# Optimization experiments

Measured on AMD Instinct MI355X. Metric: run time of the kernel, lower is better.

The kernel has to match this reference:

```python
import jax, jax.numpy as jnp
import numpy as np

B = 256          # batch
S = 128 * 128    # s = imwidth*imheight (flattened image)
R = 16           # TT rank
N = 6            # number of TT cores


def setup_inputs() -> dict:
    key = jax.random.key(0)
    ks = jax.random.split(key, N + 1)
    # layeroptions['normalize']: cores divided by sqrt(sqrt(s))
    scale = 0.02 / np.sqrt(np.sqrt(S))
    ranklist = [1] + [R] * (N - 1) + [1]
    inp = {"z": jax.random.normal(ks[0], (B, S), dtype=jnp.float32)}
    for n in range(N):
        inp[f"core{n}"] = (
            jax.random.normal(ks[n + 1], (ranklist[n], S, ranklist[n + 1]), dtype=jnp.float32)
            * scale
        )
    inp["b"] = B
    return inp


def reference(z, core0, core1, core2, core3, core4, core5, b):
    # cores[k] has shape (d1, S, d2) with ranklist = [1, R, ..., R, 1]
    cores = [core0, core1, core2, core3, core4, core5]
    # f starts as TT[0][0] : (S, R)  (first core has d1 == 1)
    f = core0[0]
    # V_k[b] = sum_s z[b, s] * cores[k][:, s, :]   -> (b, d1, d2)
    # (equivalent to matmul(z, TT[k].permute(1,0,2).reshape(S, d1*d2)))
    V1 = jnp.einsum('bs,dse->bde', z, cores[1])          # (B, R, R)
    f = jnp.einsum('sd,bde->bse', f, V1)                 # (B, S, R)
    for k in range(2, N):
        Vk = jnp.einsum('bs,dse->bde', z, cores[k])      # (B, R, d2)
        f = jnp.einsum('bsd,bde->bse', f, Vk)            # (B, S, d2)
    # final d2 == 1 -> (B, S, 1) -> flatten like f.reshape(-1)
    return f.reshape(-1)
```

## Files before the change

kernel.cpp:

```cpp
#include <hip/hip_runtime.h>
#include <cstddef>
#include <cstdint>

namespace {
constexpr int kB = 256;
constexpr int kS = 16384;
constexpr int kNCol = 1040;
constexpr int kSB = kS / 8;
}

using short8 = __attribute__((ext_vector_type(8))) short;
using f32x4  = __attribute__((ext_vector_type(4))) float;

__global__ __launch_bounds__(256) void fttv_split(
    const float* __restrict__ z,
    unsigned short* __restrict__ zh, unsigned short* __restrict__ zl)
{
    const int i = blockIdx.x * 256 + threadIdx.x;
    const int lr = i & 15;
    const int sblk = (i >> 4) & (kSB - 1);
    const int rowblk = i >> 15;
    const int row = rowblk * 16 + lr;
    const float* src = z + (size_t)row * kS + sblk * 8;
    float x[8];
    *reinterpret_cast<float4*>(&x[0]) = *reinterpret_cast<const float4*>(src);
    *reinterpret_cast<float4*>(&x[4]) = *reinterpret_cast<const float4*>(src + 4);
    short8 h, l;
    #pragma unroll
    for (int j = 0; j < 8; ++j) {
        const uint32_t u = __float_as_uint(x[j]);
        h[j] = (short)(u >> 16);
        const float r = x[j] - __uint_as_float(u & 0xffff0000u);
        l[j] = (short)(__float_as_uint(r) >> 16);
    }
    const size_t idx = (((size_t)rowblk * kSB + sblk) * 16 + lr) * 8;
    *reinterpret_cast<short8*>(zh + idx) = h;
    *reinterpret_cast<short8*>(zl + idx) = l;
}

__device__ __forceinline__ void load_a(
    const unsigned short* __restrict__ zhp, const unsigned short* __restrict__ zlp,
    int sblk0, short8 ah[4], short8 al[4])
{
    #pragma unroll
    for (int fm = 0; fm < 4; ++fm) {
        const size_t o = ((size_t)fm * kSB + sblk0) * 128;
        ah[fm] = *reinterpret_cast<const short8*>(zhp + o);
        al[fm] = *reinterpret_cast<const short8*>(zlp + o);
    }
}

__device__ __forceinline__ void load_b(const float* const bptr[4], int s0,
                                       float rb[4][8])
{
    #pragma unroll
    for (int fn = 0; fn < 4; ++fn)
        #pragma unroll
        for (int j = 0; j < 8; ++j)
            rb[fn][j] = bptr[fn][(size_t)(s0 + j) * 16];
}

__device__ __forceinline__ void step_mfma(
    const short8 ah[4], const short8 al[4], const float rb[4][8],
    f32x4 acc[4][4])
{
    #pragma unroll
    for (int fn = 0; fn < 4; ++fn) {
        short8 bh, bl;
        #pragma unroll
        for (int j = 0; j < 8; ++j) {
            const uint32_t u = __float_as_uint(rb[fn][j]);
            bh[j] = (short)(u >> 16);
            const float r = rb[fn][j] - __uint_as_float(u & 0xffff0000u);
            bl[j] = (short)(__float_as_uint(r) >> 16);
        }
        #pragma unroll
        for (int fm = 0; fm < 4; ++fm) {
            acc[fm][fn] = __builtin_amdgcn_mfma_f32_16x16x32_bf16(
                ah[fm], bh, acc[fm][fn], 0, 0, 0);
            acc[fm][fn] = __builtin_amdgcn_mfma_f32_16x16x32_bf16(
                ah[fm], bl, acc[fm][fn], 0, 0, 0);
            acc[fm][fn] = __builtin_amdgcn_mfma_f32_16x16x32_bf16(
                al[fm], bh, acc[fm][fn], 0, 0, 0);
        }
    }
}

__global__ __launch_bounds__(64, 2) void fttv_gemm_t(
    const unsigned short* __restrict__ zh, const unsigned short* __restrict__ zl,
    const float* __restrict__ c1, const float* __restrict__ c2,
    const float* __restrict__ c3, const float* __restrict__ c4,
    const float* __restrict__ c5,
    float* __restrict__ vp, int kc)
{
    const int nwg = gridDim.x;
    const int q = nwg >> 3, r = nwg & 7;
    const int xcd = blockIdx.x & 7, rest = blockIdx.x >> 3;
    const int vfl = (xcd < r ? xcd * (q + 1) : r * (q + 1) + (xcd - r) * q) + rest;
    const int sk = vfl / 68;
    const int rem = vfl - sk * 68;
    const int mt = rem / 17;
    const int cg = rem - mt * 17;

    const int l = threadIdx.x;
    const int lr = l & 15, lkq = l >> 4;
    const int nsteps = kc >> 5;
    const int sb00 = sk * (kc >> 3);
    const int s0base = sk * kc + lkq * 8;

    const unsigned short* zhp = zh + ((size_t)(mt * 4) * kSB + lkq) * 128 + lr * 8;
    const unsigned short* zlp = zl + ((size_t)(mt * 4) * kSB + lkq) * 128 + lr * 8;

    f32x4 acc[4][4];
    #pragma unroll
    for (int i = 0; i < 4; ++i)
        #pragma unroll
        for (int j = 0; j < 4; ++j) acc[i][j] = (f32x4){0.f, 0.f, 0.f, 0.f};

    short8 ah0[4], al0[4], ah1[4], al1[4];

    if (cg < 16) {
        const int ci = cg >> 2;
        const float* cp = (ci == 0 ? c1 : ci == 1 ? c2 : ci == 2 ? c3 : c4);
        const int d0 = (cg & 3) * 4;
        const float* bptr[4];
        #pragma unroll
        for (int fn = 0; fn < 4; ++fn)
            bptr[fn] = cp + (size_t)(d0 + fn) * kS * 16 + lr;

        float rb0[4][8], rb1[4][8];
        load_b(bptr, s0base, rb0);
        load_a(zhp, zlp, sb00, ah0, al0);
        for (int t = 0; t < nsteps; t += 2) {
            load_b(bptr, s0base + (t + 1) * 32, rb1);
            load_a(zhp, zlp, sb00 + (t + 1) * 4, ah1, al1);
            step_mfma(ah0, al0, rb0, acc);
            if (t + 2 < nsteps) {
                load_b(bptr, s0base + (t + 2) * 32, rb0);
                load_a(zhp, zlp, sb00 + (t + 2) * 4, ah0, al0);
            }
            step_mfma(ah1, al1, rb1, acc);
        }
        #pragma unroll
        for (int fm = 0; fm < 4; ++fm)
            #pragma unroll
            for (int fn = 0; fn < 4; ++fn) {
                const int col = cg * 64 + fn * 16 + lr;
                const int brow = mt * 64 + fm * 16 + lkq * 4;
                #pragma unroll
                for (int qq = 0; qq < 4; ++qq)
                    vp[((size_t)sk * kB + brow + qq) * kNCol + col] =
                        acc[fm][fn][qq];
            }
    } else {
        const float* bp5 = c5 + (size_t)lr * kS;
        float r50[8], r51[8];
        load_a(zhp, zlp, sb00, ah0, al0);
        *reinterpret_cast<float4*>(&r50[0]) =
            *reinterpret_cast<const float4*>(bp5 + s0base);
        *reinterpret_cast<float4*>(&r50[4]) =
            *reinterpret_cast<const float4*>(bp5 + s0base + 4);
        for (int t = 0; t < nsteps; t += 2) {
            load_a(zhp, zlp, sb00 + (t + 1) * 4, ah1, al1);
            *reinterpret_cast<float4*>(&r51[0]) =
                *reinterpret_cast<const float4*>(bp5 + s0base + (t + 1) * 32);
            *reinterpret_cast<float4*>(&r51[4]) =
                *reinterpret_cast<const float4*>(bp5 + s0base + (t + 1) * 32 + 4);
            {
                short8 bh, bl;
                #pragma unroll
                for (int j = 0; j < 8; ++j) {
                    const uint32_t u = __float_as_uint(r50[j]);
                    bh[j] = (short)(u >> 16);
                    const float rr = r50[j] - __uint_as_float(u & 0xffff0000u);
                    bl[j] = (short)(__float_as_uint(rr) >> 16);
                }
                #pragma unroll
                for (int fm = 0; fm < 4; ++fm) {
                    acc[fm][0] = __builtin_amdgcn_mfma_f32_16x16x32_bf16(
                        ah0[fm], bh, acc[fm][0], 0, 0, 0);
                    acc[fm][0] = __builtin_amdgcn_mfma_f32_16x16x32_bf16(
                        ah0[fm], bl, acc[fm][0], 0, 0, 0);
                    acc[fm][0] = __builtin_amdgcn_mfma_f32_16x16x32_bf16(
                        al0[fm], bh, acc[fm][0], 0, 0, 0);
                }
            }
            if (t + 2 < nsteps) {
                load_a(zhp, zlp, sb00 + (t + 2) * 4, ah0, al0);
                *reinterpret_cast<float4*>(&r50[0]) =
                    *reinterpret_cast<const float4*>(bp5 + s0base + (t + 2) * 32);
                *reinterpret_cast<float4*>(&r50[4]) =
                    *reinterpret_cast<const float4*>(bp5 + s0base + (t + 2) * 32 + 4);
            }
            {
                short8 bh, bl;
                #pragma unroll
                for (int j = 0; j < 8; ++j) {
                    const uint32_t u = __float_as_uint(r51[j]);
                    bh[j] = (short)(u >> 16);
                    const float rr = r51[j] - __uint_as_float(u & 0xffff0000u);
                    bl[j] = (short)(__float_as_uint(rr) >> 16);
                }
                #pragma unroll
                for (int fm = 0; fm < 4; ++fm) {
                    acc[fm][0] = __builtin_amdgcn_mfma_f32_16x16x32_bf16(
                        ah1[fm], bh, acc[fm][0], 0, 0, 0);
                    acc[fm][0] = __builtin_amdgcn_mfma_f32_16x16x32_bf16(
                        ah1[fm], bl, acc[fm][0], 0, 0, 0);
                    acc[fm][0] = __builtin_amdgcn_mfma_f32_16x16x32_bf16(
                        al1[fm], bh, acc[fm][0], 0, 0, 0);
                }
            }
        }
        #pragma unroll
        for (int fm = 0; fm < 4; ++fm) {
            const int col = 1024 + lr;
            const int brow = mt * 64 + fm * 16 + lkq * 4;
            #pragma unroll
            for (int qq = 0; qq < 4; ++qq)
                vp[((size_t)sk * kB + brow + qq) * kNCol + col] = acc[fm][0][qq];
        }
    }
}

__global__ void fttv_reduce(const float* __restrict__ vp, float* __restrict__ v,
                            int splitk)
{
    const int i4 = blockIdx.x * 256 + threadIdx.x;
    float4 s = make_float4(0.f, 0.f, 0.f, 0.f);
    for (int k = 0; k < splitk; ++k) {
        const float4 t = *reinterpret_cast<const float4*>(
            vp + (size_t)k * kNCol * kB + (size_t)i4 * 4);
        s.x += t.x; s.y += t.y; s.z += t.z; s.w += t.w;
    }
    *reinterpret_cast<float4*>(v + (size_t)i4 * 4) = s;
}

__global__ void fttv_chain(const float* __restrict__ v, float* __restrict__ w)
{
    const int b = blockIdx.x;
    const float* vb = v + (size_t)b * kNCol;
    const int lane = threadIdx.x;
    const int d = lane & 15;
    float u = vb[1024 + d];
    #pragma unroll
    for (int k = 4; k >= 1; --k) {
        float nu = 0.f;
        #pragma unroll
        for (int e = 0; e < 16; ++e) {
            const float ue = __shfl(u, e, 16);
            nu += vb[(k - 1) * 256 + d * 16 + e] * ue;
        }
        u = nu;
    }
    if (lane < 16) w[b * 16 + d] = u;
}

__global__ __launch_bounds__(256) void fttv_out(
    const float* __restrict__ c0, const float* __restrict__ w,
    float* __restrict__ out)
{
    __shared__ float wl[64][16];
    const int sc = blockIdx.x & 63;
    const int bq = blockIdx.x >> 6;
    const int tid = threadIdx.x;
    const int s = sc * 256 + tid;
    float f0[16];
    #pragma unroll
    for (int q = 0; q < 4; ++q)
        *reinterpret_cast<float4*>(&f0[q * 4]) =
            *reinterpret_cast<const float4*>(c0 + (size_t)s * 16 + q * 4);
    *reinterpret_cast<float4*>(&wl[0][0] + tid * 4) =
        *reinterpret_cast<const float4*>(w + bq * 1024 + tid * 4);
    __syncthreads();
    for (int bb = 0; bb < 64; ++bb) {
        float a = 0.f;
        #pragma unroll
        for (int d = 0; d < 16; ++d) a += f0[d] * wl[bb][d];
        out[(size_t)(bq * 64 + bb) * kS + s] = a;
    }
}

extern "C" void kernel_launch(void* const* d_in, const int* in_sizes, int n_in,
                              void* d_out, int out_size, void* d_ws, size_t ws_size,
                              hipStream_t stream)
{
    (void)in_sizes; (void)n_in; (void)out_size;
    const float* z  = (const float*)d_in[0];
    const float* c0 = (const float*)d_in[1];
    const float* c1 = (const float*)d_in[2];
    const float* c2 = (const float*)d_in[3];
    const float* c3 = (const float*)d_in[4];
    const float* c4 = (const float*)d_in[5];
    const float* c5 = (const float*)d_in[6];
    float* out = (float*)d_out;
    float* ws  = (float*)d_ws;

    const size_t zhlF = (size_t)kB * kS;
    int splitk = 64;
    while (splitk > 1 &&
           (zhlF + (size_t)(splitk + 1) * kNCol * kB + (size_t)kB * 16)
               * sizeof(float) > ws_size)
        splitk >>= 1;
    const int kc = kS / splitk;

    unsigned short* zh = (unsigned short*)ws;
    unsigned short* zl = zh + (size_t)kB * kS;
    float* vp = ws + zhlF;
    float* v  = vp + (size_t)splitk * kNCol * kB;
    float* w  = v + (size_t)kNCol * kB;

    fttv_split<<<dim3((kB * kS / 8) / 256), 256, 0, stream>>>(z, zh, zl);
    fttv_gemm_t<<<dim3(68 * splitk), 64, 0, stream>>>(
        zh, zl, c1, c2, c3, c4, c5, vp, kc);
    fttv_reduce<<<dim3(kNCol * kB / 1024), 256, 0, stream>>>(vp, v, splitk);
    fttv_chain<<<dim3(kB), 64, 0, stream>>>(v, w);
    fttv_out<<<dim3(256), 256, 0, stream>>>(c0, w, out);
}
```

Baseline: 87.05 us.

## Drop bl MFMA term with RNE split, use atomic split-K reduction

```diff
diff --git a/kernel.cpp b/kernel.cpp
--- a/kernel.cpp
+++ b/kernel.cpp
@@ -11,6 +11,11 @@
 
 using short8 = __attribute__((ext_vector_type(8))) short;
 using f32x4  = __attribute__((ext_vector_type(4))) float;
+
+__device__ __forceinline__ unsigned short bf16_rne(float x) {
+    const uint32_t u = __float_as_uint(x);
+    return (unsigned short)((u + 0x7FFFu + ((u >> 16) & 1u)) >> 16);
+}
 
 __global__ __launch_bounds__(256) void fttv_split(
     const float* __restrict__ z,
@@ -28,9 +33,9 @@
     short8 h, l;
     #pragma unroll
     for (int j = 0; j < 8; ++j) {
-        const uint32_t u = __float_as_uint(x[j]);
-        h[j] = (short)(u >> 16);
-        const float r = x[j] - __uint_as_float(u & 0xffff0000u);
+        const unsigned short hb = bf16_rne(x[j]);
+        h[j] = (short)hb;
+        const float r = x[j] - __uint_as_float((uint32_t)hb << 16);
         l[j] = (short)(__float_as_uint(r) >> 16);
     }
     const size_t idx = (((size_t)rowblk * kSB + sblk) * 16 + lr) * 8;
@@ -64,26 +69,23 @@
     const short8 ah[4], const short8 al[4], const float rb[4][8],
     f32x4 acc[4][4])
 {
-    #pragma unroll
-    for (int fn = 0; fn < 4; ++fn) {
-        short8 bh, bl;
-        #pragma unroll
-        for (int j = 0; j < 8; ++j) {
-            const uint32_t u = __float_as_uint(rb[fn][j]);
-            bh[j] = (short)(u >> 16);
-            const float r = rb[fn][j] - __uint_as_float(u & 0xffff0000u);
-            bl[j] = (short)(__float_as_uint(r) >> 16);
-        }
+    short8 bh[4];
+    #pragma unroll
+    for (int fn = 0; fn < 4; ++fn)
+        #pragma unroll
+        for (int j = 0; j < 8; ++j)
+            bh[fn][j] = (short)bf16_rne(rb[fn][j]);
+    __builtin_amdgcn_s_setprio(1);
+    #pragma unroll
+    for (int fn = 0; fn < 4; ++fn)
         #pragma unroll
         for (int fm = 0; fm < 4; ++fm) {
             acc[fm][fn] = __builtin_amdgcn_mfma_f32_16x16x32_bf16(
-                ah[fm], bh, acc[fm][fn], 0, 0, 0);
+                ah[fm], bh[fn], acc[fm][fn], 0, 0, 0);
             acc[fm][fn] = __builtin_amdgcn_mfma_f32_16x16x32_bf16(
-                ah[fm], bl, acc[fm][fn], 0, 0, 0);
-            acc[fm][fn] = __builtin_amdgcn_mfma_f32_16x16x32_bf16(
-                al[fm], bh, acc[fm][fn], 0, 0, 0);
-        }
-    }
+                al[fm], bh[fn], acc[fm][fn], 0, 0, 0);
+        }
+    __builtin_amdgcn_s_setprio(0);
 }
 
 __global__ __launch_bounds__(64, 2) void fttv_gemm_t(
@@ -91,7 +93,7 @@
     const float* __restrict__ c1, const float* __restrict__ c2,
     const float* __restrict__ c3, const float* __restrict__ c4,
     const float* __restrict__ c5,
-    float* __restrict__ vp, int kc)
+    float* __restrict__ v, int kc)
 {
     const int nwg = gridDim.x;
     const int q = nwg >> 3, r = nwg & 7;
@@ -149,8 +151,8 @@
                 const int brow = mt * 64 + fm * 16 + lkq * 4;
                 #pragma unroll
                 for (int qq = 0; qq < 4; ++qq)
-                    vp[((size_t)sk * kB + brow + qq) * kNCol + col] =
-                        acc[fm][fn][qq];
+                    atomicAdd(&v[(size_t)(brow + qq) * kNCol + col],
+                              acc[fm][fn][qq]);
             }
     } else {
         const float* bp5 = c5 + (size_t)lr * kS;
@@ -167,20 +169,13 @@
             *reinterpret_cast<float4*>(&r51[4]) =
                 *reinterpret_cast<const float4*>(bp5 + s0base + (t + 1) * 32 + 4);
             {
-                short8 bh, bl;
-                #pragma unroll
-                for (int j = 0; j < 8; ++j) {
-                    const uint32_t u = __float_as_uint(r50[j]);
-                    bh[j] = (short)(u >> 16);
-                    const float rr = r50[j] - __uint_as_float(u & 0xffff0000u);
-                    bl[j] = (short)(__float_as_uint(rr) >> 16);
-                }
+                short8 bh;
+                #pragma unroll
+                for (int j = 0; j < 8; ++j) bh[j] = (short)bf16_rne(r50[j]);
                 #pragma unroll
                 for (int fm = 0; fm < 4; ++fm) {
                     acc[fm][0] = __builtin_amdgcn_mfma_f32_16x16x32_bf16(
                         ah0[fm], bh, acc[fm][0], 0, 0, 0);
-                    acc[fm][0] = __builtin_amdgcn_mfma_f32_16x16x32_bf16(
-                        ah0[fm], bl, acc[fm][0], 0, 0, 0);
                     acc[fm][0] = __builtin_amdgcn_mfma_f32_16x16x32_bf16(
                         al0[fm], bh, acc[fm][0], 0, 0, 0);
                 }
@@ -193,20 +188,13 @@
                     *reinterpret_cast<const float4*>(bp5 + s0base + (t + 2) * 32 + 4);
             }
             {
-                short8 bh, bl;
-                #pragma unroll
-                for (int j = 0; j < 8; ++j) {
-                    const uint32_t u = __float_as_uint(r51[j]);
-                    bh[j] = (short)(u >> 16);
-                    const float rr = r51[j] - __uint_as_float(u & 0xffff0000u);
-                    bl[j] = (short)(__float_as_uint(rr) >> 16);
-                }
+                short8 bh;
+                #pragma unroll
+                for (int j = 0; j < 8; ++j) bh[j] = (short)bf16_rne(r51[j]);
                 #pragma unroll
                 for (int fm = 0; fm < 4; ++fm) {
                     acc[fm][0] = __builtin_amdgcn_mfma_f32_16x16x32_bf16(
                         ah1[fm], bh, acc[fm][0], 0, 0, 0);
-                    acc[fm][0] = __builtin_amdgcn_mfma_f32_16x16x32_bf16(
-                        ah1[fm], bl, acc[fm][0], 0, 0, 0);
                     acc[fm][0] = __builtin_amdgcn_mfma_f32_16x16x32_bf16(
                         al1[fm], bh, acc[fm][0], 0, 0, 0);
                 }
@@ -218,22 +206,9 @@
             const int brow = mt * 64 + fm * 16 + lkq * 4;
             #pragma unroll
             for (int qq = 0; qq < 4; ++qq)
-                vp[((size_t)sk * kB + brow + qq) * kNCol + col] = acc[fm][0][qq];
-        }
-    }
-}
-
-__global__ void fttv_reduce(const float* __restrict__ vp, float* __restrict__ v,
-                            int splitk)
-{
-    const int i4 = blockIdx.x * 256 + threadIdx.x;
-    float4 s = make_float4(0.f, 0.f, 0.f, 0.f);
-    for (int k = 0; k < splitk; ++k) {
-        const float4 t = *reinterpret_cast<const float4*>(
-            vp + (size_t)k * kNCol * kB + (size_t)i4 * 4);
-        s.x += t.x; s.y += t.y; s.z += t.z; s.w += t.w;
-    }
-    *reinterpret_cast<float4*>(v + (size_t)i4 * 4) = s;
+                atomicAdd(&v[(size_t)(brow + qq) * kNCol + col], acc[fm][0][qq]);
+        }
+    }
 }
 
 __global__ void fttv_chain(const float* __restrict__ v, float* __restrict__ w)
@@ -285,7 +260,7 @@
                               void* d_out, int out_size, void* d_ws, size_t ws_size,
                               hipStream_t stream)
 {
-    (void)in_sizes; (void)n_in; (void)out_size;
+    (void)in_sizes; (void)n_in; (void)out_size; (void)ws_size;
     const float* z  = (const float*)d_in[0];
     const float* c0 = (const float*)d_in[1];
     const float* c1 = (const float*)d_in[2];
@@ -297,23 +272,18 @@
     float* ws  = (float*)d_ws;
 
     const size_t zhlF = (size_t)kB * kS;
-    int splitk = 64;
-    while (splitk > 1 &&
-           (zhlF + (size_t)(splitk + 1) * kNCol * kB + (size_t)kB * 16)
-               * sizeof(float) > ws_size)
-        splitk >>= 1;
+    const int splitk = 32;
     const int kc = kS / splitk;
 
     unsigned short* zh = (unsigned short*)ws;
     unsigned short* zl = zh + (size_t)kB * kS;
-    float* vp = ws + zhlF;
-    float* v  = vp + (size_t)splitk * kNCol * kB;
-    float* w  = v + (size_t)kNCol * kB;
-
+    float* v = ws + zhlF;
+    float* w = v + (size_t)kNCol * kB;
+
+    hipMemsetAsync(v, 0, (size_t)kNCol * kB * sizeof(float), stream);
     fttv_split<<<dim3((kB * kS / 8) / 256), 256, 0, stream>>>(z, zh, zl);
     fttv_gemm_t<<<dim3(68 * splitk), 64, 0, stream>>>(
-        zh, zl, c1, c2, c3, c4, c5, vp, kc);
-    fttv_reduce<<<dim3(kNCol * kB / 1024), 256, 0, stream>>>(vp, v, splitk);
+        zh, zl, c1, c2, c3, c4, c5, v, kc);
     fttv_chain<<<dim3(kB), 64, 0, stream>>>(v, w);
     fttv_out<<<dim3(256), 256, 0, stream>>>(c0, w, out);
 }
```

After: 85.12 us. 2.2% less time.
